# Performance work log

Measured on AMD Instinct MI355X. Metric: run time of the kernel, lower is better.

The kernel has to match this reference:

```python
import jax, jax.numpy as jnp
import numpy as np

RATIO = 4   # compression ratio (group size)
H = 6       # index heads
D = 64      # index head dim = max(8, 768//6//2)
TOPK = 8    # index_topk
EPS = 1e-6  # rms_norm eps


def rms_norm(x):
    return x * jax.lax.rsqrt(jnp.mean(jnp.square(x), axis=-1, keepdims=True) + EPS)


def setup_inputs() -> dict:
    key = jax.random.key(0)
    k1, k2, k3, k4, k5 = jax.random.split(key, 5)
    B, T, E = 4, 4096, 768
    s = 0.02
    return {
        "x": jax.random.normal(k1, (B, T, E), jnp.float32),
        "wq": jax.random.normal(k2, (E, H * D), jnp.float32) * s,
        "wk": jax.random.normal(k3, (E, H * D), jnp.float32) * s,
        "wg": jax.random.normal(k4, (E, H * D), jnp.float32) * s,
        "ape": jax.random.normal(k5, (RATIO, H, D), jnp.float32) * s,
    }


def reference(x, wq, wk, wg, ape):
    B, T, E = x.shape
    G = -(-T // RATIO)          # ceil(T / ratio)
    pad = G * RATIO - T

    # --- compress keys: gated pooling over ratio-groups ---
    k = (x @ wk).reshape(B, T, H, D)
    gate = (x @ wg).reshape(B, T, H, D)
    if pad:
        k = jnp.pad(k, ((0, 0), (0, pad), (0, 0), (0, 0)))
        gate = jnp.pad(gate, ((0, 0), (0, pad), (0, 0), (0, 0)), constant_values=-jnp.inf)
    k = k.reshape(B, G, RATIO, H, D)
    gate = gate.reshape(B, G, RATIO, H, D) + ape[None, None]
    w = jax.nn.softmax(gate.astype(jnp.float32), axis=2).astype(k.dtype)
    keys = rms_norm(jnp.sum(k * w, axis=2))           # [B,G,H,D]
    group_ends = jnp.minimum(jnp.arange(RATIO - 1, G * RATIO, RATIO), T - 1)  # [G]

    # --- query-key scores ---
    q = rms_norm((x @ wq).reshape(B, T, H, D))
    scores = jnp.einsum('bthd,bghd->bhtg', q, keys) * (D ** -0.5)
    scores = jnp.mean(scores, axis=1)                 # [B,T,G]

    # --- causal mask over group ends, then top-k selection ---
    causal = group_ends[None, None, :] <= jnp.arange(T)[None, :, None]  # [1,T,G]
    scores = jnp.where(causal, scores, -jnp.inf)
    topk = min(TOPK, G)
    _, sel = jax.lax.top_k(scores, topk)              # [B,T,topk]

    # scatter selected indices into boolean mask
    bi = jnp.arange(B)[:, None, None]
    ti = jnp.arange(T)[None, :, None]
    mask = jnp.zeros((B, T, G), dtype=bool).at[bi, ti, sel].set(True)
    return (mask & causal, group_ends)
```

## Files before the change

### kernel.cpp

```cpp
#include <hip/hip_runtime.h>
#include <hip/hip_bf16.h>
#include <math.h>

#define B_    4
#define T_    4096
#define E_    768
#define H_    6
#define D_    64
#define HD_   384
#define G_    1024
#define RATIO_ 4
#define TOPK_ 8
#define MT_   (B_*T_)
#define NS_   1152

typedef __attribute__((ext_vector_type(8))) short short8;
typedef __attribute__((ext_vector_type(4))) float f32x4;
typedef __hip_bfloat16 bf16;

#define GLD16(g, l) __builtin_amdgcn_global_load_lds( \
    (const __attribute__((address_space(1))) void*)(g), \
    (__attribute__((address_space(3))) void*)(l), 16, 0, 0)

static __device__ __forceinline__ unsigned short f2bf(float f) {
  bf16 h = __float2bfloat16(f);
  return __builtin_bit_cast(unsigned short, h);
}
static __device__ __forceinline__ unsigned umax_(unsigned a, unsigned b) { return a > b ? a : b; }
static __device__ __forceinline__ unsigned umin_(unsigned a, unsigned b) { return a > b ? b : a; }

__global__ __launch_bounds__(256) void cvt_x_kernel(
    const float* __restrict__ in, bf16* __restrict__ out)
{
  size_t i = (size_t)blockIdx.x * 256 + threadIdx.x;
  const float4* p = reinterpret_cast<const float4*>(in) + i * 2;
  float4 v0 = p[0], v1 = p[1];
  float f[8] = {v0.x, v0.y, v0.z, v0.w, v1.x, v1.y, v1.z, v1.w};
  union { unsigned short u[8]; short8 v; } r;
#pragma unroll
  for (int k = 0; k < 8; ++k) r.u[k] = f2bf(f[k]);
  *reinterpret_cast<short8*>(out + i * 8) = r.v;
}

__global__ __launch_bounds__(256) void cvt_w_t(
    const float* __restrict__ wq, const float* __restrict__ wk,
    const float* __restrict__ wg, bf16* __restrict__ outbase)
{
  const int z = blockIdx.z;
  const float* src = z == 0 ? wq : (z == 1 ? wk : wg);
  __shared__ float t[32][33];
  int r = threadIdx.x >> 5, c = threadIdx.x & 31;
  int k0 = blockIdx.x * 32, n0 = blockIdx.y * 32;
#pragma unroll
  for (int i = 0; i < 4; ++i)
    t[r + i * 8][c] = src[(size_t)(k0 + r + i * 8) * HD_ + n0 + c];
  __syncthreads();
#pragma unroll
  for (int i = 0; i < 4; ++i) {
    int cc = n0 + r + i * 8;
    int ro = (z == 0) ? cc : 384 + ((cc >> 4) << 5) + ((z - 1) << 4) + (cc & 15);
    outbase[(size_t)ro * E_ + k0 + c] = __float2bfloat16(t[c][r + i * 8]);
  }
}

__global__ __launch_bounds__(256, 3) void gemm_qkg_mfma(
    const bf16* __restrict__ X, const bf16* __restrict__ Ws,
    const float* __restrict__ ape, bf16* __restrict__ Q,
    bf16* __restrict__ keys)
{
  __shared__ bf16 lds[2][8192];
  const int tid = threadIdx.x;
  const int lane = tid & 63, wv = tid >> 6;
  const int ll = lane & 15, lh = lane >> 4;
  const int m0 = blockIdx.x * 128, n0 = blockIdx.y * 128;
  const int srow = tid >> 3;
  const int sslot = (((tid & 7) ^ ((tid >> 3) & 7)) << 3);
  const bf16* pS = Ws + (size_t)(n0 + srow) * E_ + sslot;
  const bf16* pA0 = X + (size_t)(m0 + wv * 32 + ll) * E_ + lh * 8;
  const bf16* pA1 = pA0 + (size_t)16 * E_;

#define STAGE(b, k0) do { \
    char* base_ = (char*)&lds[b][0] + tid * 16; \
    GLD16(pS + (k0),            base_); \
    GLD16(pS + 32 * E_ + (k0),  base_ + 4096); \
    GLD16(pS + 64 * E_ + (k0),  base_ + 8192); \
    GLD16(pS + 96 * E_ + (k0),  base_ + 12288); \
  } while (0)
#define LOAD_A(dst, k0) do { \
    dst[0][0] = *reinterpret_cast<const short8*>(pA0 + (k0)); \
    dst[0][1] = *reinterpret_cast<const short8*>(pA0 + (k0) + 32); \
    dst[1][0] = *reinterpret_cast<const short8*>(pA1 + (k0)); \
    dst[1][1] = *reinterpret_cast<const short8*>(pA1 + (k0) + 32); \
  } while (0)

  f32x4 acc[2][8];
#pragma unroll
  for (int m = 0; m < 2; ++m)
#pragma unroll
    for (int n = 0; n < 8; ++n) acc[m][n] = (f32x4){0.f, 0.f, 0.f, 0.f};

  short8 curA[2][2], nxtA[2][2];
  LOAD_A(curA, 0);
  STAGE(0, 0);
#pragma unroll
  for (int m = 0; m < 2; ++m)
#pragma unroll
    for (int s = 0; s < 2; ++s) nxtA[m][s] = curA[m][s];

#pragma unroll
  for (int k = 0; k < 12; ++k) {
    const int k0 = k * 64;
    if (k < 11) {
      LOAD_A(nxtA, k0 + 64);
      STAGE((k + 1) & 1, k0 + 64);
    }
    if (k < 11) asm volatile("s_waitcnt vmcnt(8)" ::: "memory");
    else        asm volatile("s_waitcnt vmcnt(0)" ::: "memory");
    __builtin_amdgcn_s_barrier();
    __builtin_amdgcn_sched_barrier(0);
    const bf16* Lb = &lds[k & 1][0];
    short8 b0[8];
#pragma unroll
    for (int n = 0; n < 8; ++n)
      b0[n] = *reinterpret_cast<const short8*>(
          &Lb[(n * 16 + ll) * 64 + ((lh ^ (ll & 7)) << 3)]);
    asm volatile("s_waitcnt lgkmcnt(0)" ::: "memory");
    __builtin_amdgcn_sched_barrier(0);
#pragma unroll
    for (int m = 0; m < 2; ++m)
#pragma unroll
      for (int n = 0; n < 8; ++n)
        acc[m][n] = __builtin_amdgcn_mfma_f32_16x16x32_bf16(curA[m][0], b0[n], acc[m][n], 0, 0, 0);
    short8 b1[8];
#pragma unroll
    for (int n = 0; n < 8; ++n)
      b1[n] = *reinterpret_cast<const short8*>(
          &Lb[(n * 16 + ll) * 64 + (((4 + lh) ^ (ll & 7)) << 3)]);
    asm volatile("s_waitcnt lgkmcnt(0)" ::: "memory");
    __builtin_amdgcn_sched_barrier(0);
    __builtin_amdgcn_s_barrier();
#pragma unroll
    for (int m = 0; m < 2; ++m)
#pragma unroll
      for (int n = 0; n < 8; ++n)
        acc[m][n] = __builtin_amdgcn_mfma_f32_16x16x32_bf16(curA[m][1], b1[n], acc[m][n], 0, 0, 0);
#pragma unroll
    for (int m = 0; m < 2; ++m)
#pragma unroll
      for (int s = 0; s < 2; ++s) curA[m][s] = nxtA[m][s];
  }
#undef STAGE
#undef LOAD_A

  if (blockIdx.y < 3) {
#pragma unroll
    for (int m = 0; m < 2; ++m)
#pragma unroll
      for (int j = 0; j < 4; ++j) {
        int row = m0 + wv * 32 + m * 16 + lh * 4 + j;
#pragma unroll
        for (int h = 0; h < 2; ++h) {
          float ss = 0.f;
#pragma unroll
          for (int n = 4 * h; n < 4 * h + 4; ++n) ss += acc[m][n][j] * acc[m][n][j];
          ss += __shfl_xor(ss, 1, 64); ss += __shfl_xor(ss, 2, 64);
          ss += __shfl_xor(ss, 4, 64); ss += __shfl_xor(ss, 8, 64);
          float scl = rsqrtf(ss * (1.0f / D_) + 1e-6f);
#pragma unroll
          for (int n = 4 * h; n < 4 * h + 4; ++n)
            Q[(size_t)row * HD_ + n0 + n * 16 + ll] =
                __float2bfloat16(acc[m][n][j] * scl);
        }
      }
  } else {
    const int hcb = (n0 - 384) >> 1;
    float apev[4][4];
#pragma unroll
    for (int p = 0; p < 4; ++p) {
      int hc = hcb + p * 16 + ll;
#pragma unroll
      for (int j = 0; j < 4; ++j) apev[p][j] = ape[j * HD_ + hc];
    }
#pragma unroll
    for (int m = 0; m < 2; ++m) {
      float pooled[4];
#pragma unroll
      for (int p = 0; p < 4; ++p) {
        float g0 = acc[m][2 * p + 1][0] + apev[p][0];
        float g1 = acc[m][2 * p + 1][1] + apev[p][1];
        float g2 = acc[m][2 * p + 1][2] + apev[p][2];
        float g3 = acc[m][2 * p + 1][3] + apev[p][3];
        float mx = fmaxf(fmaxf(g0, g1), fmaxf(g2, g3));
        float e0 = expf(g0 - mx), e1 = expf(g1 - mx);
        float e2 = expf(g2 - mx), e3 = expf(g3 - mx);
        float inv = 1.0f / (e0 + e1 + e2 + e3);
        pooled[p] = (acc[m][2 * p][0] * e0 + acc[m][2 * p][1] * e1 +
                     acc[m][2 * p][2] * e2 + acc[m][2 * p][3] * e3) * inv;
      }
      float ss = pooled[0] * pooled[0] + pooled[1] * pooled[1] +
                 pooled[2] * pooled[2] + pooled[3] * pooled[3];
      ss += __shfl_xor(ss, 1, 64); ss += __shfl_xor(ss, 2, 64);
      ss += __shfl_xor(ss, 4, 64); ss += __shfl_xor(ss, 8, 64);
      float scl = rsqrtf(ss * (1.0f / D_) + 1e-6f);
      int prow = (m0 >> 2) + wv * 8 + m * 4 + lh;
#pragma unroll
      for (int p = 0; p < 4; ++p)
        keys[(size_t)prow * HD_ + hcb + p * 16 + ll] =
            __float2bfloat16(pooled[p] * scl);
    }
  }
}

__global__ __launch_bounds__(256, 4) void score_topk_fused(
    const bf16* __restrict__ Qall, const bf16* __restrict__ Kall,
    int* __restrict__ mask, int* __restrict__ ends)
{
  const int x = blockIdx.x;
  const int b = blockIdx.y;
  const int s = (b < 2) ? x : 255 - x;
  const int t0 = s << 4;
  const int tid = threadIdx.x;
  const int w = tid >> 6;
  const int lane = tid & 63;
  const int ll = lane & 15, lh = lane >> 4;

  __shared__ unsigned top[4][16][8];

  if (x == 0 && b == 0) {
    int g = tid;
#pragma unroll
    for (int c = 0; c < 4; ++c, g += 256) {
      int e = (g << 2) + 3;
      ends[g] = e < T_ - 1 ? e : T_ - 1;
    }
  }

  int* mbase = mask + ((size_t)b * T_ + t0) * G_;
  {
    int4* m4 = reinterpret_cast<int4*>(mbase);
    const int4 z = make_int4(0, 0, 0, 0);
#pragma unroll
    for (int i = 0; i < 16; ++i) m4[i * 256 + tid] = z;
  }

  const bf16* Qb = Qall + (size_t)b * T_ * HD_;
  const bf16* Kb = Kall + (size_t)b * G_ * HD_;
  const int t = t0 + ll;
  const int gmax = (t + 1) >> 2;
  const int nmega = ((t0 >> 2) + 4 + 63) >> 6;

  short8 qf[12];
  {
    const bf16* pQ = Qb + (size_t)t * HD_ + lh * 8;
#pragma unroll
    for (int k = 0; k < 12; ++k)
      qf[k] = *reinterpret_cast<const short8*>(pQ + k * 32);
  }

  unsigned v0 = 0, v1 = 0, v2 = 0, v3 = 0, v4 = 0, v5 = 0, v6 = 0, v7 = 0;
#define INS(xx) do { unsigned k_ = (xx), t_; \
    t_ = umax_(v0, k_); k_ = umin_(v0, k_); v0 = t_; \
    t_ = umax_(v1, k_); k_ = umin_(v1, k_); v1 = t_; \
    t_ = umax_(v2, k_); k_ = umin_(v2, k_); v2 = t_; \
    t_ = umax_(v3, k_); k_ = umin_(v3, k_); v3 = t_; \
    t_ = umax_(v4, k_); k_ = umin_(v4, k_); v4 = t_; \
    t_ = umax_(v5, k_); k_ = umin_(v5, k_); v5 = t_; \
    t_ = umax_(v6, k_); k_ = umin_(v6, k_); v6 = t_; \
    t_ = umax_(v7, k_); k_ = umin_(v7, k_); v7 = t_; } while (0)

  for (int mg = w; mg < nmega; mg += 4) {
    const int g0 = mg << 6;
    const bf16* pK = Kb + (size_t)(g0 + ll) * HD_ + lh * 8;
    short8 kf[12][4];
#pragma unroll
    for (int kk = 0; kk < 12; ++kk)
#pragma unroll
      for (int tl = 0; tl < 4; ++tl)
        kf[kk][tl] = *reinterpret_cast<const short8*>(
            pK + (size_t)tl * 16 * HD_ + kk * 32);
    f32x4 acc[4];
#pragma unroll
    for (int tl = 0; tl < 4; ++tl) acc[tl] = (f32x4){0.f, 0.f, 0.f, 0.f};
#pragma unroll
    for (int kk = 0; kk < 12; ++kk)
#pragma unroll
      for (int tl = 0; tl < 4; ++tl)
        acc[tl] = __builtin_amdgcn_mfma_f32_16x16x32_bf16(
            kf[kk][tl], qf[kk], acc[tl], 0, 0, 0);
#pragma unroll
    for (int tl = 0; tl < 4; ++tl)
#pragma unroll
      for (int j = 0; j < 4; ++j) {
        int g = g0 + tl * 16 + lh * 4 + j;
        float xv = acc[tl][j] + 512.0f;
        unsigned key = (g < gmax)
            ? ((__builtin_bit_cast(unsigned, xv) & 0xFFFFFC00u) |
               (unsigned)(1023 - g))
            : 0u;
        INS(key);
      }
  }
#undef INS

#define CEx(a, bb) { unsigned h_ = umax_(a, bb), l_ = umin_(a, bb); a = h_; bb = l_; }
#define MERGE4() \
  _Pragma("unroll") \
  for (int st = 0; st < 2; ++st) { \
    const int off = 16 << st; \
    unsigned p0 = (unsigned)__shfl_xor((int)v0, off, 64); \
    unsigned p1 = (unsigned)__shfl_xor((int)v1, off, 64); \
    unsigned p2 = (unsigned)__shfl_xor((int)v2, off, 64); \
    unsigned p3 = (unsigned)__shfl_xor((int)v3, off, 64); \
    unsigned p4 = (unsigned)__shfl_xor((int)v4, off, 64); \
    unsigned p5 = (unsigned)__shfl_xor((int)v5, off, 64); \
    unsigned p6 = (unsigned)__shfl_xor((int)v6, off, 64); \
    unsigned p7 = (unsigned)__shfl_xor((int)v7, off, 64); \
    unsigned w0 = umax_(v0, p7), w1 = umax_(v1, p6); \
    unsigned w2 = umax_(v2, p5), w3 = umax_(v3, p4); \
    unsigned w4 = umax_(v4, p3), w5 = umax_(v5, p2); \
    unsigned w6 = umax_(v6, p1), w7 = umax_(v7, p0); \
    CEx(w0, w4); CEx(w1, w5); CEx(w2, w6); CEx(w3, w7); \
    CEx(w0, w2); CEx(w1, w3); CEx(w4, w6); CEx(w5, w7); \
    CEx(w0, w1); CEx(w2, w3); CEx(w4, w5); CEx(w6, w7); \
    v0 = w0; v1 = w1; v2 = w2; v3 = w3; v4 = w4; v5 = w5; v6 = w6; v7 = w7; \
  }

  MERGE4();

  if (lh == 0) {
    unsigned* tp = &top[w][ll][0];
    tp[0] = v0; tp[1] = v1; tp[2] = v2; tp[3] = v3;
    tp[4] = v4; tp[5] = v5; tp[6] = v6; tp[7] = v7;
  }
  __syncthreads();

  if (w == 0) {
    const unsigned* tp = &top[lh][ll][0];
    v0 = tp[0]; v1 = tp[1]; v2 = tp[2]; v3 = tp[3];
    v4 = tp[4]; v5 = tp[5]; v6 = tp[6]; v7 = tp[7];
    MERGE4();
    if (lh == 0) {
      int* rb = mbase + (size_t)ll * G_;
      if (v0) rb[1023 - (v0 & 1023)] = 1;
      if (v1) rb[1023 - (v1 & 1023)] = 1;
      if (v2) rb[1023 - (v2 & 1023)] = 1;
      if (v3) rb[1023 - (v3 & 1023)] = 1;
      if (v4) rb[1023 - (v4 & 1023)] = 1;
      if (v5) rb[1023 - (v5 & 1023)] = 1;
      if (v6) rb[1023 - (v6 & 1023)] = 1;
      if (v7) rb[1023 - (v7 & 1023)] = 1;
    }
  }
#undef MERGE4
#undef CEx
}

extern "C" void kernel_launch(void* const* d_in, const int* in_sizes, int n_in,
                              void* d_out, int out_size, void* d_ws, size_t ws_size,
                              hipStream_t stream)
{
  const float* x   = (const float*)d_in[0];
  const float* wq  = (const float*)d_in[1];
  const float* wk  = (const float*)d_in[2];
  const float* wg  = (const float*)d_in[3];
  const float* ape = (const float*)d_in[4];

  bf16* Ws   = (bf16*)d_ws;
  bf16* qb   = Ws + (size_t)NS_ * E_;
  bf16* keys = qb + (size_t)MT_ * HD_;

  bf16* xb = (bf16*)d_out;

  cvt_x_kernel<<<dim3(MT_ * E_ / 8 / 256), dim3(256), 0, stream>>>(x, xb);
  cvt_w_t<<<dim3(E_ / 32, HD_ / 32, 3), dim3(256), 0, stream>>>(wq, wk, wg, Ws);

  gemm_qkg_mfma<<<dim3(MT_ / 128, NS_ / 128), dim3(256), 0, stream>>>(
      xb, Ws, ape, qb, keys);

  score_topk_fused<<<dim3(256, B_), dim3(256), 0, stream>>>(
      qb, keys, (int*)d_out, (int*)d_out + (size_t)B_ * T_ * G_);
}
```

Measured before the change: 120.3 us.

## Stage Q in LDS and overlap top-k insertion with split K loads

Q fragments are now staged into shared memory once per block and read per k-step instead of being held in 12 registers. The K fragment loads are split into two halves, and the previous megablock's top-k insertion runs between the second-half loads and their MFMAs to hide load latency. Occupancy is lowered from 4 to 3 waves per SIMD in launch bounds to allow more registers. The cost is extra LDS traffic, a block-wide sync, and a 16-entry candidate buffer held in registers.

```diff
diff --git a/kernel.cpp b/kernel.cpp
--- a/kernel.cpp
+++ b/kernel.cpp
@@ -211,7 +211,7 @@
   }
 }
 
-__global__ __launch_bounds__(256, 4) void score_topk_fused(
+__global__ __launch_bounds__(256, 3) void score_topk_fused(
     const bf16* __restrict__ Qall, const bf16* __restrict__ Kall,
     int* __restrict__ mask, int* __restrict__ ends)
 {
@@ -224,6 +224,7 @@
   const int lane = tid & 63;
   const int ll = lane & 15, lh = lane >> 4;
 
+  __shared__ short qls[48 * 16 * 8];
   __shared__ unsigned top[4][16][8];
 
   if (x == 0 && b == 0) {
@@ -245,19 +246,27 @@
 
   const bf16* Qb = Qall + (size_t)b * T_ * HD_;
   const bf16* Kb = Kall + (size_t)b * G_ * HD_;
-  const int t = t0 + ll;
-  const int gmax = (t + 1) >> 2;
+  const int gmax = (t0 + ll + 1) >> 2;
   const int nmega = ((t0 >> 2) + 4 + 63) >> 6;
 
-  short8 qf[12];
   {
-    const bf16* pQ = Qb + (size_t)t * HD_ + lh * 8;
-#pragma unroll
-    for (int k = 0; k < 12; ++k)
-      qf[k] = *reinterpret_cast<const short8*>(pQ + k * 32);
-  }
+    const int r = tid >> 4, c0 = tid & 15;
+#pragma unroll
+    for (int it = 0; it < 3; ++it) {
+      int c = c0 + 16 * it;
+      short8 qv = *reinterpret_cast<const short8*>(
+          Qb + (size_t)(t0 + r) * HD_ + c * 8);
+      *reinterpret_cast<short8*>(
+          reinterpret_cast<char*>(qls) + c * 256 + r * 16) = qv;
+    }
+  }
+  __syncthreads();
+  const char* qbase = reinterpret_cast<const char*>(qls) + ll * 16;
 
   unsigned v0 = 0, v1 = 0, v2 = 0, v3 = 0, v4 = 0, v5 = 0, v6 = 0, v7 = 0;
+  unsigned cp[16];
+  int have = 0;
+
 #define INS(xx) do { unsigned k_ = (xx), t_; \
     t_ = umax_(v0, k_); k_ = umin_(v0, k_); v0 = t_; \
     t_ = umax_(v1, k_); k_ = umin_(v1, k_); v1 = t_; \
@@ -271,34 +280,62 @@
   for (int mg = w; mg < nmega; mg += 4) {
     const int g0 = mg << 6;
     const bf16* pK = Kb + (size_t)(g0 + ll) * HD_ + lh * 8;
-    short8 kf[12][4];
-#pragma unroll
-    for (int kk = 0; kk < 12; ++kk)
+    f32x4 acc[4];
+#pragma unroll
+    for (int tl = 0; tl < 4; ++tl) acc[tl] = (f32x4){0.f, 0.f, 0.f, 0.f};
+
+    short8 kf[6][4];
+#pragma unroll
+    for (int kk = 0; kk < 6; ++kk)
 #pragma unroll
       for (int tl = 0; tl < 4; ++tl)
         kf[kk][tl] = *reinterpret_cast<const short8*>(
             pK + (size_t)tl * 16 * HD_ + kk * 32);
-    f32x4 acc[4];
-#pragma unroll
-    for (int tl = 0; tl < 4; ++tl) acc[tl] = (f32x4){0.f, 0.f, 0.f, 0.f};
-#pragma unroll
-    for (int kk = 0; kk < 12; ++kk)
+    __builtin_amdgcn_sched_barrier(0);
+#pragma unroll
+    for (int kk = 0; kk < 6; ++kk) {
+      short8 qv = *reinterpret_cast<const short8*>(
+          qbase + (kk * 4 + lh) * 256);
 #pragma unroll
       for (int tl = 0; tl < 4; ++tl)
-        acc[tl] = __builtin_amdgcn_mfma_f32_16x16x32_bf16(
-            kf[kk][tl], qf[kk], acc[tl], 0, 0, 0);
+        acc[tl] = __builtin_amdgcn_mfma_f32_16x16x32_bf16(kf[kk][tl], qv, acc[tl], 0, 0, 0);
+    }
+#pragma unroll
+    for (int kk = 0; kk < 6; ++kk)
+#pragma unroll
+      for (int tl = 0; tl < 4; ++tl)
+        kf[kk][tl] = *reinterpret_cast<const short8*>(
+            pK + (size_t)tl * 16 * HD_ + (kk + 6) * 32);
+    __builtin_amdgcn_sched_barrier(0);
+    if (have) {
+#pragma unroll
+      for (int i = 0; i < 16; ++i) INS(cp[i]);
+    }
+    __builtin_amdgcn_sched_barrier(0);
+#pragma unroll
+    for (int kk = 0; kk < 6; ++kk) {
+      short8 qv = *reinterpret_cast<const short8*>(
+          qbase + ((kk + 6) * 4 + lh) * 256);
+#pragma unroll
+      for (int tl = 0; tl < 4; ++tl)
+        acc[tl] = __builtin_amdgcn_mfma_f32_16x16x32_bf16(kf[kk][tl], qv, acc[tl], 0, 0, 0);
+    }
 #pragma unroll
     for (int tl = 0; tl < 4; ++tl)
 #pragma unroll
       for (int j = 0; j < 4; ++j) {
         int g = g0 + tl * 16 + lh * 4 + j;
         float xv = acc[tl][j] + 512.0f;
-        unsigned key = (g < gmax)
+        cp[tl * 4 + j] = (g < gmax)
             ? ((__builtin_bit_cast(unsigned, xv) & 0xFFFFFC00u) |
                (unsigned)(1023 - g))
             : 0u;
-        INS(key);
       }
+    have = 1;
+  }
+  if (have) {
+#pragma unroll
+    for (int i = 0; i < 16; ++i) INS(cp[i]);
   }
 #undef INS
 
```

Result: slower. 135.0 us (+12.2%).

## Split score/top-k into partial per-quarter kernel and separate mask-write merge kernel

Applied to the files above, without the earlier changes.

The fused score+top-k kernel becomes two kernels. The first launches four times as many blocks, each handling one quarter of the key mega-tiles for a 16-row slice, and writes partial top-8 lists to workspace. The second merges the four partials, zeroes the mask, and scatters the selected indices. The goal is better load balance and occupancy for the causal, triangular workload, and keeping the mask-zeroing stores out of the compute kernel. The cost is an extra launch and a workspace round trip for the partials.

```diff
diff --git a/kernel.cpp b/kernel.cpp
--- a/kernel.cpp
+++ b/kernel.cpp
@@ -210,97 +210,6 @@
     }
   }
 }
-
-__global__ __launch_bounds__(256, 4) void score_topk_fused(
-    const bf16* __restrict__ Qall, const bf16* __restrict__ Kall,
-    int* __restrict__ mask, int* __restrict__ ends)
-{
-  const int x = blockIdx.x;
-  const int b = blockIdx.y;
-  const int s = (b < 2) ? x : 255 - x;
-  const int t0 = s << 4;
-  const int tid = threadIdx.x;
-  const int w = tid >> 6;
-  const int lane = tid & 63;
-  const int ll = lane & 15, lh = lane >> 4;
-
-  __shared__ unsigned top[4][16][8];
-
-  if (x == 0 && b == 0) {
-    int g = tid;
-#pragma unroll
-    for (int c = 0; c < 4; ++c, g += 256) {
-      int e = (g << 2) + 3;
-      ends[g] = e < T_ - 1 ? e : T_ - 1;
-    }
-  }
-
-  int* mbase = mask + ((size_t)b * T_ + t0) * G_;
-  {
-    int4* m4 = reinterpret_cast<int4*>(mbase);
-    const int4 z = make_int4(0, 0, 0, 0);
-#pragma unroll
-    for (int i = 0; i < 16; ++i) m4[i * 256 + tid] = z;
-  }
-
-  const bf16* Qb = Qall + (size_t)b * T_ * HD_;
-  const bf16* Kb = Kall + (size_t)b * G_ * HD_;
-  const int t = t0 + ll;
-  const int gmax = (t + 1) >> 2;
-  const int nmega = ((t0 >> 2) + 4 + 63) >> 6;
-
-  short8 qf[12];
-  {
-    const bf16* pQ = Qb + (size_t)t * HD_ + lh * 8;
-#pragma unroll
-    for (int k = 0; k < 12; ++k)
-      qf[k] = *reinterpret_cast<const short8*>(pQ + k * 32);
-  }
-
-  unsigned v0 = 0, v1 = 0, v2 = 0, v3 = 0, v4 = 0, v5 = 0, v6 = 0, v7 = 0;
-#define INS(xx) do { unsigned k_ = (xx), t_; \
-    t_ = umax_(v0, k_); k_ = umin_(v0, k_); v0 = t_; \
-    t_ = umax_(v1, k_); k_ = umin_(v1, k_); v1 = t_; \
-    t_ = umax_(v2, k_); k_ = umin_(v2, k_); v2 = t_; \
-    t_ = umax_(v3, k_); k_ = umin_(v3, k_); v3 = t_; \
-    t_ = umax_(v4, k_); k_ = umin_(v4, k_); v4 = t_; \
-    t_ = umax_(v5, k_); k_ = umin_(v5, k_); v5 = t_; \
-    t_ = umax_(v6, k_); k_ = umin_(v6, k_); v6 = t_; \
-    t_ = umax_(v7, k_); k_ = umin_(v7, k_); v7 = t_; } while (0)
-
-  for (int mg = w; mg < nmega; mg += 4) {
-    const int g0 = mg << 6;
-    const bf16* pK = Kb + (size_t)(g0 + ll) * HD_ + lh * 8;
-    short8 kf[12][4];
-#pragma unroll
-    for (int kk = 0; kk < 12; ++kk)
-#pragma unroll
-      for (int tl = 0; tl < 4; ++tl)
-        kf[kk][tl] = *reinterpret_cast<const short8*>(
-            pK + (size_t)tl * 16 * HD_ + kk * 32);
-    f32x4 acc[4];
-#pragma unroll
-    for (int tl = 0; tl < 4; ++tl) acc[tl] = (f32x4){0.f, 0.f, 0.f, 0.f};
-#pragma unroll
-    for (int kk = 0; kk < 12; ++kk)
-#pragma unroll
-      for (int tl = 0; tl < 4; ++tl)
-        acc[tl] = __builtin_amdgcn_mfma_f32_16x16x32_bf16(
-            kf[kk][tl], qf[kk], acc[tl], 0, 0, 0);
-#pragma unroll
-    for (int tl = 0; tl < 4; ++tl)
-#pragma unroll
-      for (int j = 0; j < 4; ++j) {
-        int g = g0 + tl * 16 + lh * 4 + j;
-        float xv = acc[tl][j] + 512.0f;
-        unsigned key = (g < gmax)
-            ? ((__builtin_bit_cast(unsigned, xv) & 0xFFFFFC00u) |
-               (unsigned)(1023 - g))
-            : 0u;
-        INS(key);
-      }
-  }
-#undef INS
 
 #define CEx(a, bb) { unsigned h_ = umax_(a, bb), l_ = umin_(a, bb); a = h_; bb = l_; }
 #define MERGE4() \
@@ -325,6 +234,79 @@
     v0 = w0; v1 = w1; v2 = w2; v3 = w3; v4 = w4; v5 = w5; v6 = w6; v7 = w7; \
   }
 
+__global__ __launch_bounds__(256, 4) void score_partial(
+    const bf16* __restrict__ Qall, const bf16* __restrict__ Kall,
+    unsigned* __restrict__ part)
+{
+  const int x = blockIdx.x;
+  const int b = blockIdx.y;
+  const int s = x >> 2, qtr = x & 3;
+  const int t0 = s << 4;
+  const int tid = threadIdx.x;
+  const int w = tid >> 6;
+  const int lane = tid & 63;
+  const int ll = lane & 15, lh = lane >> 4;
+
+  __shared__ unsigned top[4][16][8];
+
+  const bf16* Qb = Qall + (size_t)b * T_ * HD_;
+  const bf16* Kb = Kall + (size_t)b * G_ * HD_;
+  const int t = t0 + ll;
+  const int gmax = (t + 1) >> 2;
+  const int nmega = ((t0 >> 2) + 4 + 63) >> 6;
+  const int mg = qtr + 4 * w;
+
+  unsigned v0 = 0, v1 = 0, v2 = 0, v3 = 0, v4 = 0, v5 = 0, v6 = 0, v7 = 0;
+#define INS(xx) do { unsigned k_ = (xx), t_; \
+    t_ = umax_(v0, k_); k_ = umin_(v0, k_); v0 = t_; \
+    t_ = umax_(v1, k_); k_ = umin_(v1, k_); v1 = t_; \
+    t_ = umax_(v2, k_); k_ = umin_(v2, k_); v2 = t_; \
+    t_ = umax_(v3, k_); k_ = umin_(v3, k_); v3 = t_; \
+    t_ = umax_(v4, k_); k_ = umin_(v4, k_); v4 = t_; \
+    t_ = umax_(v5, k_); k_ = umin_(v5, k_); v5 = t_; \
+    t_ = umax_(v6, k_); k_ = umin_(v6, k_); v6 = t_; \
+    t_ = umax_(v7, k_); k_ = umin_(v7, k_); v7 = t_; } while (0)
+
+  if (mg < nmega) {
+    short8 qf[12];
+    const bf16* pQ = Qb + (size_t)t * HD_ + lh * 8;
+#pragma unroll
+    for (int k = 0; k < 12; ++k)
+      qf[k] = *reinterpret_cast<const short8*>(pQ + k * 32);
+
+    const int g0 = mg << 6;
+    const bf16* pK = Kb + (size_t)(g0 + ll) * HD_ + lh * 8;
+    short8 kf[12][4];
+#pragma unroll
+    for (int kk = 0; kk < 12; ++kk)
+#pragma unroll
+      for (int tl = 0; tl < 4; ++tl)
+        kf[kk][tl] = *reinterpret_cast<const short8*>(
+            pK + (size_t)tl * 16 * HD_ + kk * 32);
+    f32x4 acc[4];
+#pragma unroll
+    for (int tl = 0; tl < 4; ++tl) acc[tl] = (f32x4){0.f, 0.f, 0.f, 0.f};
+#pragma unroll
+    for (int kk = 0; kk < 12; ++kk)
+#pragma unroll
+      for (int tl = 0; tl < 4; ++tl)
+        acc[tl] = __builtin_amdgcn_mfma_f32_16x16x32_bf16(
+            kf[kk][tl], qf[kk], acc[tl], 0, 0, 0);
+#pragma unroll
+    for (int tl = 0; tl < 4; ++tl)
+#pragma unroll
+      for (int j = 0; j < 4; ++j) {
+        int g = g0 + tl * 16 + lh * 4 + j;
+        float xv = acc[tl][j] + 512.0f;
+        unsigned key = (g < gmax)
+            ? ((__builtin_bit_cast(unsigned, xv) & 0xFFFFFC00u) |
+               (unsigned)(1023 - g))
+            : 0u;
+        INS(key);
+      }
+  }
+#undef INS
+
   MERGE4();
 
   if (lh == 0) {
@@ -340,19 +322,60 @@
     v4 = tp[4]; v5 = tp[5]; v6 = tp[6]; v7 = tp[7];
     MERGE4();
     if (lh == 0) {
-      int* rb = mbase + (size_t)ll * G_;
-      if (v0) rb[1023 - (v0 & 1023)] = 1;
-      if (v1) rb[1023 - (v1 & 1023)] = 1;
-      if (v2) rb[1023 - (v2 & 1023)] = 1;
-      if (v3) rb[1023 - (v3 & 1023)] = 1;
-      if (v4) rb[1023 - (v4 & 1023)] = 1;
-      if (v5) rb[1023 - (v5 & 1023)] = 1;
-      if (v6) rb[1023 - (v6 & 1023)] = 1;
-      if (v7) rb[1023 - (v7 & 1023)] = 1;
+      unsigned* pp = part + ((((size_t)b * 256 + s) * 4 + qtr) * 16 + ll) * 8;
+      reinterpret_cast<int4*>(pp)[0] = make_int4((int)v0, (int)v1, (int)v2, (int)v3);
+      reinterpret_cast<int4*>(pp)[1] = make_int4((int)v4, (int)v5, (int)v6, (int)v7);
     }
   }
-#undef MERGE4
-#undef CEx
+}
+
+__global__ __launch_bounds__(256) void mask_write(
+    const unsigned* __restrict__ part, int* __restrict__ mask,
+    int* __restrict__ ends)
+{
+  const int tid = threadIdx.x;
+  if (blockIdx.x == 0) {
+    int g = tid;
+#pragma unroll
+    for (int c = 0; c < 4; ++c, g += 256) {
+      int e = (g << 2) + 3;
+      ends[g] = e < T_ - 1 ? e : T_ - 1;
+    }
+  }
+  const int w = tid >> 6, lane = tid & 63;
+  const int ll = lane & 15, lh = lane >> 4;
+  const int gs = blockIdx.x * 4 + w;
+  const int b = gs >> 8, s = gs & 255;
+
+  const unsigned* pp = part + ((((size_t)b * 256 + s) * 4 + lh) * 16 + ll) * 8;
+  int4 q0 = reinterpret_cast<const int4*>(pp)[0];
+  int4 q1 = reinterpret_cast<const int4*>(pp)[1];
+  unsigned v0 = (unsigned)q0.x, v1 = (unsigned)q0.y;
+  unsigned v2 = (unsigned)q0.z, v3 = (unsigned)q0.w;
+  unsigned v4 = (unsigned)q1.x, v5 = (unsigned)q1.y;
+  unsigned v6 = (unsigned)q1.z, v7 = (unsigned)q1.w;
+
+  MERGE4();
+
+  int* mbase = mask + ((size_t)b * T_ + (size_t)s * 16) * G_;
+  const int4 z = make_int4(0, 0, 0, 0);
+#pragma unroll
+  for (int r = 0; r < 16; ++r)
+#pragma unroll
+    for (int c = 0; c < 4; ++c)
+      *reinterpret_cast<int4*>(mbase + (size_t)r * G_ + (lane << 4) + (c << 2)) = z;
+  asm volatile("s_waitcnt vmcnt(0)" ::: "memory");
+  if (lh == 0) {
+    int* rb = mbase + (size_t)ll * G_;
+    if (v0) rb[1023 - (v0 & 1023)] = 1;
+    if (v1) rb[1023 - (v1 & 1023)] = 1;
+    if (v2) rb[1023 - (v2 & 1023)] = 1;
+    if (v3) rb[1023 - (v3 & 1023)] = 1;
+    if (v4) rb[1023 - (v4 & 1023)] = 1;
+    if (v5) rb[1023 - (v5 & 1023)] = 1;
+    if (v6) rb[1023 - (v6 & 1023)] = 1;
+    if (v7) rb[1023 - (v7 & 1023)] = 1;
+  }
 }
 
 extern "C" void kernel_launch(void* const* d_in, const int* in_sizes, int n_in,
@@ -368,6 +391,7 @@
   bf16* Ws   = (bf16*)d_ws;
   bf16* qb   = Ws + (size_t)NS_ * E_;
   bf16* keys = qb + (size_t)MT_ * HD_;
+  unsigned* part = (unsigned*)(keys + (size_t)B_ * G_ * HD_);
 
   bf16* xb = (bf16*)d_out;
 
@@ -377,6 +401,8 @@
   gemm_qkg_mfma<<<dim3(MT_ / 128, NS_ / 128), dim3(256), 0, stream>>>(
       xb, Ws, ape, qb, keys);
 
-  score_topk_fused<<<dim3(256, B_), dim3(256), 0, stream>>>(
-      qb, keys, (int*)d_out, (int*)d_out + (size_t)B_ * T_ * G_);
-}
+  score_partial<<<dim3(1024, B_), dim3(256), 0, stream>>>(qb, keys, part);
+
+  mask_write<<<dim3(256), dim3(256), 0, stream>>>(
+      part, (int*)d_out, (int*)d_out + (size_t)B_ * T_ * G_);
+}
```

After: 158.1 us. 1.31x slower.

## Stage keys through double-buffered LDS and split mask write into separate kernel

Applied to the files above, without the earlier changes.

The score kernel now copies key tiles into double-buffered, XOR-swizzled shared memory with async global-to-LDS loads, so the waves in a block share them. Each wave owns 16 query rows and keeps its top-8 in registers, and the per-row results go to a workspace buffer. A separate kernel then zeroes the mask, scatters the selected indices and writes group ends. This cuts redundant global key loads, but the mask zeroing no longer overlaps the score computation and there is an extra launch.

```diff
diff --git a/kernel.cpp b/kernel.cpp
--- a/kernel.cpp
+++ b/kernel.cpp
@@ -210,97 +210,6 @@
     }
   }
 }
-
-__global__ __launch_bounds__(256, 4) void score_topk_fused(
-    const bf16* __restrict__ Qall, const bf16* __restrict__ Kall,
-    int* __restrict__ mask, int* __restrict__ ends)
-{
-  const int x = blockIdx.x;
-  const int b = blockIdx.y;
-  const int s = (b < 2) ? x : 255 - x;
-  const int t0 = s << 4;
-  const int tid = threadIdx.x;
-  const int w = tid >> 6;
-  const int lane = tid & 63;
-  const int ll = lane & 15, lh = lane >> 4;
-
-  __shared__ unsigned top[4][16][8];
-
-  if (x == 0 && b == 0) {
-    int g = tid;
-#pragma unroll
-    for (int c = 0; c < 4; ++c, g += 256) {
-      int e = (g << 2) + 3;
-      ends[g] = e < T_ - 1 ? e : T_ - 1;
-    }
-  }
-
-  int* mbase = mask + ((size_t)b * T_ + t0) * G_;
-  {
-    int4* m4 = reinterpret_cast<int4*>(mbase);
-    const int4 z = make_int4(0, 0, 0, 0);
-#pragma unroll
-    for (int i = 0; i < 16; ++i) m4[i * 256 + tid] = z;
-  }
-
-  const bf16* Qb = Qall + (size_t)b * T_ * HD_;
-  const bf16* Kb = Kall + (size_t)b * G_ * HD_;
-  const int t = t0 + ll;
-  const int gmax = (t + 1) >> 2;
-  const int nmega = ((t0 >> 2) + 4 + 63) >> 6;
-
-  short8 qf[12];
-  {
-    const bf16* pQ = Qb + (size_t)t * HD_ + lh * 8;
-#pragma unroll
-    for (int k = 0; k < 12; ++k)
-      qf[k] = *reinterpret_cast<const short8*>(pQ + k * 32);
-  }
-
-  unsigned v0 = 0, v1 = 0, v2 = 0, v3 = 0, v4 = 0, v5 = 0, v6 = 0, v7 = 0;
-#define INS(xx) do { unsigned k_ = (xx), t_; \
-    t_ = umax_(v0, k_); k_ = umin_(v0, k_); v0 = t_; \
-    t_ = umax_(v1, k_); k_ = umin_(v1, k_); v1 = t_; \
-    t_ = umax_(v2, k_); k_ = umin_(v2, k_); v2 = t_; \
-    t_ = umax_(v3, k_); k_ = umin_(v3, k_); v3 = t_; \
-    t_ = umax_(v4, k_); k_ = umin_(v4, k_); v4 = t_; \
-    t_ = umax_(v5, k_); k_ = umin_(v5, k_); v5 = t_; \
-    t_ = umax_(v6, k_); k_ = umin_(v6, k_); v6 = t_; \
-    t_ = umax_(v7, k_); k_ = umin_(v7, k_); v7 = t_; } while (0)
-
-  for (int mg = w; mg < nmega; mg += 4) {
-    const int g0 = mg << 6;
-    const bf16* pK = Kb + (size_t)(g0 + ll) * HD_ + lh * 8;
-    short8 kf[12][4];
-#pragma unroll
-    for (int kk = 0; kk < 12; ++kk)
-#pragma unroll
-      for (int tl = 0; tl < 4; ++tl)
-        kf[kk][tl] = *reinterpret_cast<const short8*>(
-            pK + (size_t)tl * 16 * HD_ + kk * 32);
-    f32x4 acc[4];
-#pragma unroll
-    for (int tl = 0; tl < 4; ++tl) acc[tl] = (f32x4){0.f, 0.f, 0.f, 0.f};
-#pragma unroll
-    for (int kk = 0; kk < 12; ++kk)
-#pragma unroll
-      for (int tl = 0; tl < 4; ++tl)
-        acc[tl] = __builtin_amdgcn_mfma_f32_16x16x32_bf16(
-            kf[kk][tl], qf[kk], acc[tl], 0, 0, 0);
-#pragma unroll
-    for (int tl = 0; tl < 4; ++tl)
-#pragma unroll
-      for (int j = 0; j < 4; ++j) {
-        int g = g0 + tl * 16 + lh * 4 + j;
-        float xv = acc[tl][j] + 512.0f;
-        unsigned key = (g < gmax)
-            ? ((__builtin_bit_cast(unsigned, xv) & 0xFFFFFC00u) |
-               (unsigned)(1023 - g))
-            : 0u;
-        INS(key);
-      }
-  }
-#undef INS
 
 #define CEx(a, bb) { unsigned h_ = umax_(a, bb), l_ = umin_(a, bb); a = h_; bb = l_; }
 #define MERGE4() \
@@ -325,34 +234,157 @@
     v0 = w0; v1 = w1; v2 = w2; v3 = w3; v4 = w4; v5 = w5; v6 = w6; v7 = w7; \
   }
 
+__global__ __launch_bounds__(128, 2) void score_topk8(
+    const bf16* __restrict__ Qall, const bf16* __restrict__ Kall,
+    unsigned* __restrict__ fin)
+{
+  __shared__ bf16 kbuf[2][12288];
+  const int x = blockIdx.x;
+  const int b = blockIdx.y;
+  const int s = (b < 2) ? x : 127 - x;
+  const int R0 = s << 5;
+  const int tid = threadIdx.x;
+  const int w = tid >> 6;
+  const int lane = tid & 63;
+  const int ll = lane & 15, lh = lane >> 4;
+
+  const bf16* Qb = Qall + (size_t)b * T_ * HD_;
+  const bf16* Kb = Kall + (size_t)b * G_ * HD_;
+  const int t = R0 + 16 * w + ll;
+  const int gmax = (t + 1) >> 2;
+  const int ntw = ((((R0 + 16 * w) >> 2) + 4) + 31) >> 5;
+  const int nt  = ((((R0 + 16) >> 2) + 4) + 31) >> 5;
+
+  const bf16* ksrc[12];
+  int sdst[12];
+#pragma unroll
+  for (int i = 0; i < 12; ++i) {
+    int u = (12 * w + i) * 64 + lane;
+    int r = u / 48, sp = u - r * 48;
+    int sl = sp ^ (r & 7);
+    ksrc[i] = Kb + (size_t)r * HD_ + sl * 8;
+    sdst[i] = u * 16;
+  }
+  short8 qf[12];
+  {
+    const bf16* pQ = Qb + (size_t)t * HD_ + lh * 8;
+#pragma unroll
+    for (int k = 0; k < 12; ++k)
+      qf[k] = *reinterpret_cast<const short8*>(pQ + k * 32);
+  }
+
+#define KSTAGE(bf, g0) do { \
+    char* bb_ = (char*)&kbuf[bf][0]; \
+    _Pragma("unroll") \
+    for (int i = 0; i < 12; ++i) \
+      GLD16(ksrc[i] + (size_t)(g0) * HD_, bb_ + sdst[i]); \
+  } while (0)
+
+  unsigned v0 = 0, v1 = 0, v2 = 0, v3 = 0, v4 = 0, v5 = 0, v6 = 0, v7 = 0;
+#define INS(xx) do { unsigned k_ = (xx), t_; \
+    t_ = umax_(v0, k_); k_ = umin_(v0, k_); v0 = t_; \
+    t_ = umax_(v1, k_); k_ = umin_(v1, k_); v1 = t_; \
+    t_ = umax_(v2, k_); k_ = umin_(v2, k_); v2 = t_; \
+    t_ = umax_(v3, k_); k_ = umin_(v3, k_); v3 = t_; \
+    t_ = umax_(v4, k_); k_ = umin_(v4, k_); v4 = t_; \
+    t_ = umax_(v5, k_); k_ = umin_(v5, k_); v5 = t_; \
+    t_ = umax_(v6, k_); k_ = umin_(v6, k_); v6 = t_; \
+    t_ = umax_(v7, k_); k_ = umin_(v7, k_); v7 = t_; } while (0)
+
+  KSTAGE(0, 0);
+  for (int mg = 0; mg < nt; ++mg) {
+    if (mg + 1 < nt) {
+      KSTAGE((mg + 1) & 1, (mg + 1) * 32);
+      asm volatile("s_waitcnt vmcnt(12)" ::: "memory");
+    } else {
+      asm volatile("s_waitcnt vmcnt(0)" ::: "memory");
+    }
+    __builtin_amdgcn_s_barrier();
+    __builtin_amdgcn_sched_barrier(0);
+    if (mg < ntw) {
+      const char* Lb = (const char*)&kbuf[mg & 1][0];
+      f32x4 acc0 = (f32x4){0.f, 0.f, 0.f, 0.f};
+      f32x4 acc1 = (f32x4){0.f, 0.f, 0.f, 0.f};
+#pragma unroll
+      for (int kk = 0; kk < 12; ++kk) {
+        int sl = 4 * kk + lh;
+        short8 k0 = *reinterpret_cast<const short8*>(
+            Lb + (size_t)ll * 768 + ((sl ^ (ll & 7)) << 4));
+        short8 k1 = *reinterpret_cast<const short8*>(
+            Lb + (size_t)(16 + ll) * 768 + ((sl ^ (ll & 7)) << 4));
+        acc0 = __builtin_amdgcn_mfma_f32_16x16x32_bf16(k0, qf[kk], acc0, 0, 0, 0);
+        acc1 = __builtin_amdgcn_mfma_f32_16x16x32_bf16(k1, qf[kk], acc1, 0, 0, 0);
+      }
+      const int g0 = mg * 32;
+#pragma unroll
+      for (int j = 0; j < 4; ++j) {
+        int g = g0 + lh * 4 + j;
+        float xv = acc0[j] + 512.0f;
+        unsigned key = (g < gmax)
+            ? ((__builtin_bit_cast(unsigned, xv) & 0xFFFFFC00u) |
+               (unsigned)(1023 - g))
+            : 0u;
+        INS(key);
+      }
+#pragma unroll
+      for (int j = 0; j < 4; ++j) {
+        int g = g0 + 16 + lh * 4 + j;
+        float xv = acc1[j] + 512.0f;
+        unsigned key = (g < gmax)
+            ? ((__builtin_bit_cast(unsigned, xv) & 0xFFFFFC00u) |
+               (unsigned)(1023 - g))
+            : 0u;
+        INS(key);
+      }
+    }
+    __builtin_amdgcn_s_barrier();
+  }
+#undef INS
+#undef KSTAGE
+
   MERGE4();
 
   if (lh == 0) {
-    unsigned* tp = &top[w][ll][0];
-    tp[0] = v0; tp[1] = v1; tp[2] = v2; tp[3] = v3;
-    tp[4] = v4; tp[5] = v5; tp[6] = v6; tp[7] = v7;
-  }
+    unsigned* pp = fin + ((size_t)b * T_ + R0 + 16 * w + ll) * 8;
+    reinterpret_cast<int4*>(pp)[0] = make_int4((int)v0, (int)v1, (int)v2, (int)v3);
+    reinterpret_cast<int4*>(pp)[1] = make_int4((int)v4, (int)v5, (int)v6, (int)v7);
+  }
+}
+
+__global__ __launch_bounds__(256) void mask_write(
+    const unsigned* __restrict__ fin, int* __restrict__ mask,
+    int* __restrict__ ends)
+{
+  const int tid = threadIdx.x;
+  if (blockIdx.x == 0) {
+    int g = tid;
+#pragma unroll
+    for (int c = 0; c < 4; ++c, g += 256) {
+      int e = (g << 2) + 3;
+      ends[g] = e < T_ - 1 ? e : T_ - 1;
+    }
+  }
+  const size_t RB = (size_t)blockIdx.x * 64;
+  int4* m4 = reinterpret_cast<int4*>(mask + RB * G_);
+  const int4 z = make_int4(0, 0, 0, 0);
+#pragma unroll
+  for (int r = 0; r < 64; ++r) m4[r * 256 + tid] = z;
+  asm volatile("s_waitcnt vmcnt(0)" ::: "memory");
   __syncthreads();
-
-  if (w == 0) {
-    const unsigned* tp = &top[lh][ll][0];
-    v0 = tp[0]; v1 = tp[1]; v2 = tp[2]; v3 = tp[3];
-    v4 = tp[4]; v5 = tp[5]; v6 = tp[6]; v7 = tp[7];
-    MERGE4();
-    if (lh == 0) {
-      int* rb = mbase + (size_t)ll * G_;
-      if (v0) rb[1023 - (v0 & 1023)] = 1;
-      if (v1) rb[1023 - (v1 & 1023)] = 1;
-      if (v2) rb[1023 - (v2 & 1023)] = 1;
-      if (v3) rb[1023 - (v3 & 1023)] = 1;
-      if (v4) rb[1023 - (v4 & 1023)] = 1;
-      if (v5) rb[1023 - (v5 & 1023)] = 1;
-      if (v6) rb[1023 - (v6 & 1023)] = 1;
-      if (v7) rb[1023 - (v7 & 1023)] = 1;
-    }
-  }
-#undef MERGE4
-#undef CEx
+  if (tid < 64) {
+    const unsigned* pp = fin + (RB + tid) * 8;
+    int4 q0 = reinterpret_cast<const int4*>(pp)[0];
+    int4 q1 = reinterpret_cast<const int4*>(pp)[1];
+    int* rb = mask + (RB + tid) * G_;
+    if (q0.x) rb[1023 - ((unsigned)q0.x & 1023)] = 1;
+    if (q0.y) rb[1023 - ((unsigned)q0.y & 1023)] = 1;
+    if (q0.z) rb[1023 - ((unsigned)q0.z & 1023)] = 1;
+    if (q0.w) rb[1023 - ((unsigned)q0.w & 1023)] = 1;
+    if (q1.x) rb[1023 - ((unsigned)q1.x & 1023)] = 1;
+    if (q1.y) rb[1023 - ((unsigned)q1.y & 1023)] = 1;
+    if (q1.z) rb[1023 - ((unsigned)q1.z & 1023)] = 1;
+    if (q1.w) rb[1023 - ((unsigned)q1.w & 1023)] = 1;
+  }
 }
 
 extern "C" void kernel_launch(void* const* d_in, const int* in_sizes, int n_in,
@@ -368,6 +400,7 @@
   bf16* Ws   = (bf16*)d_ws;
   bf16* qb   = Ws + (size_t)NS_ * E_;
   bf16* keys = qb + (size_t)MT_ * HD_;
+  unsigned* fin = (unsigned*)(keys + (size_t)B_ * G_ * HD_);
 
   bf16* xb = (bf16*)d_out;
 
@@ -377,6 +410,8 @@
   gemm_qkg_mfma<<<dim3(MT_ / 128, NS_ / 128), dim3(256), 0, stream>>>(
       xb, Ws, ape, qb, keys);
 
-  score_topk_fused<<<dim3(256, B_), dim3(256), 0, stream>>>(
-      qb, keys, (int*)d_out, (int*)d_out + (size_t)B_ * T_ * G_);
-}
+  score_topk8<<<dim3(128, B_), dim3(128), 0, stream>>>(qb, keys, fin);
+
+  mask_write<<<dim3(256), dim3(256), 0, stream>>>(
+      fin, (int*)d_out, (int*)d_out + (size_t)B_ * T_ * G_);
+}
```

New measurement: 108.3 us. 1.11x faster.
